# Performance work log

Hardware: AMD Instinct MI355X
Metric: run time of the kernel (lower is better)

The kernel has to match this reference:

```python
import jax, jax.numpy as jnp
import numpy as np

N_NODES = 4096
N_EDGES = 100000
N_PAIRS = 1000000
MAX_PATH = 5
EDGE_DIM = 16


def setup_inputs() -> dict:
    key = jax.random.key(0)
    k1, k2, k3, k4, k5, k6 = jax.random.split(key, 6)
    x = jax.random.normal(k1, (N_NODES, EDGE_DIM), dtype=jnp.float32)
    edge_attr = jax.random.normal(k2, (N_EDGES, EDGE_DIM), dtype=jnp.float32)
    edge_vector = jax.random.normal(k3, (MAX_PATH, EDGE_DIM), dtype=jnp.float32)
    # unique (src, dst) pairs so the scatter-set is well-defined (matches the
    # dict-of-dicts edge_paths, where each (src, dst) appears at most once)
    pair_ids = jax.random.permutation(k4, N_NODES * N_NODES)[:N_PAIRS]
    src_idx = (pair_ids // N_NODES).astype(jnp.int64)
    dst_idx = (pair_ids % N_NODES).astype(jnp.int64)
    # ragged paths: random length in [1, MAX_PATH], padded with -1
    path_idx = jax.random.randint(k5, (N_PAIRS, MAX_PATH), 0, N_EDGES).astype(jnp.int64)
    lengths = jax.random.randint(k6, (N_PAIRS, 1), 1, MAX_PATH + 1)
    valid = jnp.arange(MAX_PATH)[None, :] < lengths
    path_idx = jnp.where(valid, path_idx, -1)
    return {"x": x, "edge_attr": edge_attr, "edge_vector": edge_vector,
            "src_idx": src_idx, "dst_idx": dst_idx, "path_idx": path_idx}


def reference(x, edge_attr, edge_vector, src_idx, dst_idx, path_idx):
    # path_idx: [P, L] edge indices, -1 = padding beyond the path length
    n = x.shape[0]
    mask = path_idx >= 0                                   # [P, L]
    safe = jnp.where(mask, path_idx, 0)
    feats = edge_attr[safe]                                # [P, L, D] irregular gather
    dots = jnp.einsum('pld,ld->pl', feats, edge_vector)    # per-hop dot products
    dots = jnp.where(mask, dots, 0.0)
    cnt = mask.sum(axis=-1)                                # path lengths
    # mean over the path; empty path -> 0 (matches nan_to_num on 0/0)
    vals = jnp.where(cnt > 0, dots.sum(axis=-1) / jnp.maximum(cnt, 1).astype(dots.dtype), 0.0)
    cij = jnp.zeros((n, n), dtype=x.dtype).at[src_idx, dst_idx].set(vals)
    return cij
```

## Files before the change

kernel.cpp:

```cpp
#include <hip/hip_runtime.h>

#define N_NODES  4096
#define MAX_PATH 5
#define EDGE_DIM 16

typedef int   iv2 __attribute__((ext_vector_type(2)));
typedef float fv2 __attribute__((ext_vector_type(2)));
typedef float fv4 __attribute__((ext_vector_type(4)));

#define BLOCK 256
#define FILL_BLOCKS 2048

__global__ __launch_bounds__(256) void fill_zero_kernel(float* __restrict__ out)
{
    const size_t nvec   = (size_t)N_NODES * N_NODES / 4;
    const size_t stride = (size_t)FILL_BLOCKS * BLOCK;
    fv4 z = {0.f, 0.f, 0.f, 0.f};
    fv4* o4 = (fv4*)out;
    for (size_t i = (size_t)blockIdx.x * BLOCK + threadIdx.x; i < nvec; i += stride)
        o4[i] = z;
}

__global__ __launch_bounds__(256) void precompute_dots_kernel(
    const float* __restrict__ edge_attr,
    const float* __restrict__ edge_vector,
    float*       __restrict__ D,
    int n_edges)
{
    int e = blockIdx.x * blockDim.x + threadIdx.x;
    if (e >= n_edges) return;

    const float4* ea = (const float4*)(edge_attr + (size_t)e * EDGE_DIM);
    float4 a0 = ea[0], a1 = ea[1], a2 = ea[2], a3 = ea[3];

#pragma unroll
    for (int l = 0; l < MAX_PATH; ++l) {
        const float4* ev = (const float4*)(edge_vector + l * EDGE_DIM);
        float4 b0 = ev[0], b1 = ev[1], b2 = ev[2], b3 = ev[3];
        float d = a0.x*b0.x + a0.y*b0.y + a0.z*b0.z + a0.w*b0.w
                + a1.x*b1.x + a1.y*b1.y + a1.z*b1.z + a1.w*b1.w
                + a2.x*b2.x + a2.y*b2.y + a2.z*b2.z + a2.w*b2.w
                + a3.x*b3.x + a3.y*b3.y + a3.z*b3.z + a3.w*b3.w;
        D[(size_t)l * n_edges + e] = d;
    }
}

__global__ __launch_bounds__(256) void gather_vals_kernel(
    const float* __restrict__ D,
    const int*   __restrict__ path_idx,
    float*       __restrict__ vals,
    int n_pairs, int n_edges)
{
    int t  = blockIdx.x * blockDim.x + threadIdx.x;
    int p0 = t * 2;
    if (p0 >= n_pairs) return;

    const iv2* pp = (const iv2*)(path_idx + (size_t)p0 * MAX_PATH);
    iv2 w0 = pp[0], w1 = pp[1], w2 = pp[2], w3 = pp[3], w4 = pp[4];
    int e[10] = { w0.x, w0.y, w1.x, w1.y, w2.x,
                  w2.y, w3.x, w3.y, w4.x, w4.y };

    float g[10];
#pragma unroll
    for (int j = 0; j < 2; ++j) {
#pragma unroll
        for (int l = 0; l < MAX_PATH; ++l) {
            int idx = e[j * MAX_PATH + l];
            g[j * MAX_PATH + l] = (idx >= 0) ? D[(size_t)l * n_edges + idx] : 0.0f;
        }
    }

    fv2 v;
#pragma unroll
    for (int j = 0; j < 2; ++j) {
        float sum = 0.0f;
        int   cnt = 0;
#pragma unroll
        for (int l = 0; l < MAX_PATH; ++l) {
            if (e[j * MAX_PATH + l] >= 0) { sum += g[j * MAX_PATH + l]; ++cnt; }
        }
        v[j] = (cnt > 0) ? (sum / (float)cnt) : 0.0f;
    }
    *(fv2*)(vals + p0) = v;
}

__global__ __launch_bounds__(256) void scatter_vals_kernel(
    const float* __restrict__ vals,
    const int*   __restrict__ src_idx,
    const int*   __restrict__ dst_idx,
    float*       __restrict__ out,
    int n_pairs)
{
    int t  = blockIdx.x * blockDim.x + threadIdx.x;
    int p0 = t * 4;
    if (p0 >= n_pairs) return;

    if (p0 + 3 < n_pairs) {
        float4 v  = *(const float4*)(vals + p0);
        int4   sv = *(const int4*)(src_idx + p0);
        int4   dv = *(const int4*)(dst_idx + p0);
        out[(size_t)sv.x * N_NODES + dv.x] = v.x;
        out[(size_t)sv.y * N_NODES + dv.y] = v.y;
        out[(size_t)sv.z * N_NODES + dv.z] = v.z;
        out[(size_t)sv.w * N_NODES + dv.w] = v.w;
    } else {
        for (int p = p0; p < n_pairs; ++p)
            out[(size_t)src_idx[p] * N_NODES + dst_idx[p]] = vals[p];
    }
}

extern "C" void kernel_launch(void* const* d_in, const int* in_sizes, int n_in,
                              void* d_out, int out_size, void* d_ws, size_t ws_size,
                              hipStream_t stream)
{
    const float* edge_attr   = (const float*)d_in[1];
    const float* edge_vector = (const float*)d_in[2];
    const int*   src_idx     = (const int*)d_in[3];
    const int*   dst_idx     = (const int*)d_in[4];
    const int*   path_idx    = (const int*)d_in[5];
    float*       out         = (float*)d_out;

    const int n_edges = in_sizes[1] / EDGE_DIM;
    const int n_pairs = in_sizes[3];

    float* D    = (float*)d_ws;
    float* vals = (float*)((char*)d_ws +
                  (((size_t)5 * n_edges * sizeof(float) + 1023) & ~(size_t)1023));

    fill_zero_kernel<<<FILL_BLOCKS, BLOCK, 0, stream>>>(out);

    precompute_dots_kernel<<<(n_edges + BLOCK - 1) / BLOCK, BLOCK, 0, stream>>>(
        edge_attr, edge_vector, D, n_edges);

    const int tA = (n_pairs + 1) / 2;
    gather_vals_kernel<<<(tA + BLOCK - 1) / BLOCK, BLOCK, 0, stream>>>(
        D, path_idx, vals, n_pairs, n_edges);

    const int tB = (n_pairs + 3) / 4;
    scatter_vals_kernel<<<(tB + BLOCK - 1) / BLOCK, BLOCK, 0, stream>>>(
        vals, src_idx, dst_idx, out, n_pairs);
}
```

Before: 53.56 us.

## Fuse output zero-fill with path gather in one interleaved launch

Merges the zero-fill kernel and the path-gather kernel into a single launch whose blocks alternate between filling the 64MB output and computing per-pair means. The write-heavy fill and the latency-bound random gather can then share the GPU at the same time, and one kernel launch plus one serialization point go away. It also adds a scalar tail path for an odd pair count. The cost is divergent block roles, and the fill blocks compete with the gather for memory bandwidth.

Result: slower. 55.79 us (+4.2%).

```diff
diff --git a/kernel.cpp b/kernel.cpp
--- a/kernel.cpp
+++ b/kernel.cpp
@@ -8,20 +8,10 @@
 typedef float fv2 __attribute__((ext_vector_type(2)));
 typedef float fv4 __attribute__((ext_vector_type(4)));
 
-#define BLOCK 256
+#define BLOCK       256
 #define FILL_BLOCKS 2048
 
-__global__ __launch_bounds__(256) void fill_zero_kernel(float* __restrict__ out)
-{
-    const size_t nvec   = (size_t)N_NODES * N_NODES / 4;
-    const size_t stride = (size_t)FILL_BLOCKS * BLOCK;
-    fv4 z = {0.f, 0.f, 0.f, 0.f};
-    fv4* o4 = (fv4*)out;
-    for (size_t i = (size_t)blockIdx.x * BLOCK + threadIdx.x; i < nvec; i += stride)
-        o4[i] = z;
-}
-
-__global__ __launch_bounds__(256) void precompute_dots_kernel(
+__global__ __launch_bounds__(256) void precompute_kernel(
     const float* __restrict__ edge_attr,
     const float* __restrict__ edge_vector,
     float*       __restrict__ D,
@@ -45,43 +35,76 @@
     }
 }
 
-__global__ __launch_bounds__(256) void gather_vals_kernel(
+__global__ __launch_bounds__(256) void fill_gather_kernel(
     const float* __restrict__ D,
     const int*   __restrict__ path_idx,
     float*       __restrict__ vals,
-    int n_pairs, int n_edges)
+    float*       __restrict__ out,
+    int n_pairs, int n_edges, int n_gather_blocks)
 {
-    int t  = blockIdx.x * blockDim.x + threadIdx.x;
+    const int bid     = (int)blockIdx.x;
+    const int nPaired = 2 * (FILL_BLOCKS < n_gather_blocks ? FILL_BLOCKS
+                                                           : n_gather_blocks);
+    bool isFill;
+    int  rid;
+    if (bid < nPaired) { isFill = ((bid & 1) == 0); rid = bid >> 1; }
+    else if (FILL_BLOCKS > n_gather_blocks) { isFill = true;  rid = n_gather_blocks + (bid - nPaired); }
+    else                                    { isFill = false; rid = FILL_BLOCKS     + (bid - nPaired); }
+
+    if (isFill) {
+        const size_t nvec   = (size_t)N_NODES * N_NODES / 4;
+        const size_t stride = (size_t)FILL_BLOCKS * BLOCK;
+        fv4 z = {0.f, 0.f, 0.f, 0.f};
+        fv4* o4 = (fv4*)out;
+        for (size_t i = (size_t)rid * BLOCK + threadIdx.x; i < nvec; i += stride)
+            o4[i] = z;
+        return;
+    }
+
+    int t  = rid * BLOCK + (int)threadIdx.x;
     int p0 = t * 2;
     if (p0 >= n_pairs) return;
 
-    const iv2* pp = (const iv2*)(path_idx + (size_t)p0 * MAX_PATH);
-    iv2 w0 = pp[0], w1 = pp[1], w2 = pp[2], w3 = pp[3], w4 = pp[4];
-    int e[10] = { w0.x, w0.y, w1.x, w1.y, w2.x,
-                  w2.y, w3.x, w3.y, w4.x, w4.y };
+    if (p0 + 1 < n_pairs) {
+        const iv2* pp = (const iv2*)(path_idx + (size_t)p0 * MAX_PATH);
+        iv2 w0 = pp[0], w1 = pp[1], w2 = pp[2], w3 = pp[3], w4 = pp[4];
+        int e[10] = { w0.x, w0.y, w1.x, w1.y, w2.x,
+                      w2.y, w3.x, w3.y, w4.x, w4.y };
 
-    float g[10];
+        float g[10];
 #pragma unroll
-    for (int j = 0; j < 2; ++j) {
+        for (int j = 0; j < 2; ++j) {
 #pragma unroll
-        for (int l = 0; l < MAX_PATH; ++l) {
-            int idx = e[j * MAX_PATH + l];
-            g[j * MAX_PATH + l] = (idx >= 0) ? D[(size_t)l * n_edges + idx] : 0.0f;
+            for (int l = 0; l < MAX_PATH; ++l) {
+                int idx = e[j * MAX_PATH + l];
+                g[j * MAX_PATH + l] = (idx >= 0) ? D[(size_t)l * n_edges + idx] : 0.0f;
+            }
+        }
+
+        fv2 v;
+#pragma unroll
+        for (int j = 0; j < 2; ++j) {
+            float sum = 0.0f;
+            int   cnt = 0;
+#pragma unroll
+            for (int l = 0; l < MAX_PATH; ++l) {
+                if (e[j * MAX_PATH + l] >= 0) { sum += g[j * MAX_PATH + l]; ++cnt; }
+            }
+            v[j] = (cnt > 0) ? (sum / (float)cnt) : 0.0f;
+        }
+        *(fv2*)(vals + p0) = v;
+    } else {
+        for (int p = p0; p < n_pairs; ++p) {
+            float sum = 0.0f;
+            int   cnt = 0;
+#pragma unroll
+            for (int l = 0; l < MAX_PATH; ++l) {
+                int idx = path_idx[(size_t)p * MAX_PATH + l];
+                if (idx >= 0) { sum += D[(size_t)l * n_edges + idx]; ++cnt; }
+            }
+            vals[p] = (cnt > 0) ? (sum / (float)cnt) : 0.0f;
         }
     }
-
-    fv2 v;
-#pragma unroll
-    for (int j = 0; j < 2; ++j) {
-        float sum = 0.0f;
-        int   cnt = 0;
-#pragma unroll
-        for (int l = 0; l < MAX_PATH; ++l) {
-            if (e[j * MAX_PATH + l] >= 0) { sum += g[j * MAX_PATH + l]; ++cnt; }
-        }
-        v[j] = (cnt > 0) ? (sum / (float)cnt) : 0.0f;
-    }
-    *(fv2*)(vals + p0) = v;
 }
 
 __global__ __launch_bounds__(256) void scatter_vals_kernel(
@@ -127,16 +150,15 @@
     float* vals = (float*)((char*)d_ws +
                   (((size_t)5 * n_edges * sizeof(float) + 1023) & ~(size_t)1023));
 
-    fill_zero_kernel<<<FILL_BLOCKS, BLOCK, 0, stream>>>(out);
-
-    precompute_dots_kernel<<<(n_edges + BLOCK - 1) / BLOCK, BLOCK, 0, stream>>>(
+    precompute_kernel<<<(n_edges + BLOCK - 1) / BLOCK, BLOCK, 0, stream>>>(
         edge_attr, edge_vector, D, n_edges);
 
-    const int tA = (n_pairs + 1) / 2;
-    gather_vals_kernel<<<(tA + BLOCK - 1) / BLOCK, BLOCK, 0, stream>>>(
-        D, path_idx, vals, n_pairs, n_edges);
+    const int tG = (n_pairs + 1) / 2;
+    const int n_gather_blocks = (tG + BLOCK - 1) / BLOCK;
+    fill_gather_kernel<<<FILL_BLOCKS + n_gather_blocks, BLOCK, 0, stream>>>(
+        D, path_idx, vals, out, n_pairs, n_edges, n_gather_blocks);
 
-    const int tB = (n_pairs + 3) / 4;
-    scatter_vals_kernel<<<(tB + BLOCK - 1) / BLOCK, BLOCK, 0, stream>>>(
+    const int tS = (n_pairs + 3) / 4;
+    scatter_vals_kernel<<<(tS + BLOCK - 1) / BLOCK, BLOCK, 0, stream>>>(
         vals, src_idx, dst_idx, out, n_pairs);
 }
```
